# Kernel tuning notes

Measured on AMD Instinct MI355X. Metric: run time of the kernel, lower is better.

The kernel has to match this reference:

```python
import jax, jax.numpy as jnp
import numpy as np

NUM_TOKENS = 32000
BATCH = 8192
K = 10  # 'ten-hot'

def setup_inputs() -> dict:
    key = jax.random.key(0)
    x = jax.random.randint(key, (BATCH, K), 0, NUM_TOKENS, dtype=jnp.int64)
    return {"x": x}

def reference(x) -> jnp.ndarray:
    # Multi-hot encode: out[n, x[n, j]] = 1 for all j. Duplicate indices simply
    # re-write 1 (set, not add), matching the torch assignment semantics.
    B = x.shape[0]
    out = jnp.zeros((B, NUM_TOKENS), dtype=jnp.float32)
    rows = jnp.arange(B, dtype=x.dtype)[:, None]  # [B,1] broadcasts over K
    out = out.at[rows, x].set(1.0, mode="drop")
    return out
```

## Files before the change

### kernel.cpp

```cpp
#include <hip/hip_runtime.h>


#define NUM_TOKENS 32000
#define KHOT 10
#define F4_PER_ROW (NUM_TOKENS / 4)
#define BLOCK 256

typedef float f32x4 __attribute__((ext_vector_type(4)));

__global__ __launch_bounds__(BLOCK) void TenHotEncodeLayer_53566832115799_kernel(
    const int* __restrict__ x, float* __restrict__ out) {
    const int row = blockIdx.x;

    int      c[KHOT];
    unsigned bit[KHOT];
    #pragma unroll
    for (int j = 0; j < KHOT; ++j) {
        const int idx = x[row * KHOT + j];
        const bool ok = (idx >= 0) && (idx < NUM_TOKENS);
        c[j]   = ok ? (idx >> 2) : -1;
        bit[j] = 1u << (idx & 3);
    }

    f32x4* __restrict__ rowp = reinterpret_cast<f32x4*>(out) + (size_t)row * F4_PER_ROW;

    #pragma unroll 1
    for (int i0 = threadIdx.x; i0 < F4_PER_ROW; i0 += 2 * BLOCK) {
        #pragma unroll
        for (int u = 0; u < 2; ++u) {
            const int i = i0 + u * BLOCK;
            if (i < F4_PER_ROW) {
                unsigned m = 0u;
                #pragma unroll
                for (int j = 0; j < KHOT; ++j) {
                    m |= (c[j] == i) ? bit[j] : 0u;
                }
                f32x4 v;
                v.x = (m & 1u) ? 1.0f : 0.0f;
                v.y = (m & 2u) ? 1.0f : 0.0f;
                v.z = (m & 4u) ? 1.0f : 0.0f;
                v.w = (m & 8u) ? 1.0f : 0.0f;
                __builtin_nontemporal_store(v, &rowp[i]);
            }
        }
    }
}

extern "C" void kernel_launch(void* const* d_in, const int* in_sizes, int n_in,
                              void* d_out, int out_size, void* d_ws, size_t ws_size,
                              hipStream_t stream) {
    const int* x = (const int*)d_in[0];
    float* out = (float*)d_out;
    const int B = in_sizes[0] / KHOT;
    TenHotEncodeLayer_53566832115799_kernel<<<B, BLOCK, 0, stream>>>(x, out);
}
```

Before: 203.5 us.

## Use fixed grid with 32 rows per block and prefetch next row's indices

Launches a fixed grid of 256 blocks, each writing 32 consecutive rows, in place of one block per row. The next row's indices are loaded while the current row is being written, hiding their load latency. This is meant to cut block launch and scheduling overhead and the per-row index-load stall. In exchange only 256 blocks feed a GPU with many CUs, which may limit occupancy and write bandwidth, and the hard-coded grid only covers all rows when B equals 8192.

```diff
diff --git a/kernel.cpp b/kernel.cpp
--- a/kernel.cpp
+++ b/kernel.cpp
@@ -5,44 +5,61 @@
 #define KHOT 10
 #define F4_PER_ROW (NUM_TOKENS / 4)
 #define BLOCK 256
+#define GRID 256
+#define ROWS_PER_BLOCK 32
 
 typedef float f32x4 __attribute__((ext_vector_type(4)));
 
 __global__ __launch_bounds__(BLOCK) void TenHotEncodeLayer_53566832115799_kernel(
-    const int* __restrict__ x, float* __restrict__ out) {
-    const int row = blockIdx.x;
+    const int* __restrict__ x, float* __restrict__ out, int B) {
+    const int row0 = blockIdx.x * ROWS_PER_BLOCK;
 
-    int      c[KHOT];
-    unsigned bit[KHOT];
+    int raw[KHOT];
     #pragma unroll
     for (int j = 0; j < KHOT; ++j) {
-        const int idx = x[row * KHOT + j];
-        const bool ok = (idx >= 0) && (idx < NUM_TOKENS);
-        c[j]   = ok ? (idx >> 2) : -1;
-        bit[j] = 1u << (idx & 3);
+        const int rr = (row0 < B) ? row0 : 0;
+        raw[j] = x[rr * KHOT + j];
     }
 
-    f32x4* __restrict__ rowp = reinterpret_cast<f32x4*>(out) + (size_t)row * F4_PER_ROW;
+    for (int r = 0; r < ROWS_PER_BLOCK; ++r) {
+        const int row = row0 + r;
+        if (row >= B) break;
 
-    #pragma unroll 1
-    for (int i0 = threadIdx.x; i0 < F4_PER_ROW; i0 += 2 * BLOCK) {
+        int      c[KHOT];
+        unsigned bit[KHOT];
         #pragma unroll
-        for (int u = 0; u < 2; ++u) {
-            const int i = i0 + u * BLOCK;
-            if (i < F4_PER_ROW) {
-                unsigned m = 0u;
-                #pragma unroll
-                for (int j = 0; j < KHOT; ++j) {
-                    m |= (c[j] == i) ? bit[j] : 0u;
-                }
-                f32x4 v;
-                v.x = (m & 1u) ? 1.0f : 0.0f;
-                v.y = (m & 2u) ? 1.0f : 0.0f;
-                v.z = (m & 4u) ? 1.0f : 0.0f;
-                v.w = (m & 8u) ? 1.0f : 0.0f;
-                __builtin_nontemporal_store(v, &rowp[i]);
+        for (int j = 0; j < KHOT; ++j) {
+            const int idx = raw[j];
+            const bool ok = (idx >= 0) && (idx < NUM_TOKENS);
+            c[j]   = ok ? (idx >> 2) : -1;
+            bit[j] = 1u << (idx & 3);
+        }
+
+        int nxt[KHOT];
+        {
+            const int rn = (row + 1 < B) ? (row + 1) : row;
+            #pragma unroll
+            for (int j = 0; j < KHOT; ++j) nxt[j] = x[rn * KHOT + j];
+        }
+
+        f32x4* __restrict__ rowp =
+            reinterpret_cast<f32x4*>(out) + (size_t)row * F4_PER_ROW;
+        for (int i = threadIdx.x; i < F4_PER_ROW; i += BLOCK) {
+            unsigned m = 0u;
+            #pragma unroll
+            for (int j = 0; j < KHOT; ++j) {
+                m |= (c[j] == i) ? bit[j] : 0u;
             }
+            f32x4 v;
+            v.x = (m & 1u) ? 1.0f : 0.0f;
+            v.y = (m & 2u) ? 1.0f : 0.0f;
+            v.z = (m & 4u) ? 1.0f : 0.0f;
+            v.w = (m & 8u) ? 1.0f : 0.0f;
+            __builtin_nontemporal_store(v, &rowp[i]);
         }
+
+        #pragma unroll
+        for (int j = 0; j < KHOT; ++j) raw[j] = nxt[j];
     }
 }
 
@@ -52,5 +69,5 @@
     const int* x = (const int*)d_in[0];
     float* out = (float*)d_out;
     const int B = in_sizes[0] / KHOT;
-    TenHotEncodeLayer_53566832115799_kernel<<<B, BLOCK, 0, stream>>>(x, out);
+    TenHotEncodeLayer_53566832115799_kernel<<<GRID, BLOCK, 0, stream>>>(x, out, B);
 }
```

New measurement: 236.1 us. 1.16x slower.

## Switch to persistent grid-stride flat fill with prefetched row indices

Applied to the files above, without the earlier changes.

Replaces the one-block-per-row launch (8192 blocks) with a fixed 256-block grid that walks the flat output in a grid-stride loop. Each thread computes its row and column per element and prefetches the next iteration's ten indices, so the index loads overlap the current store. It also swaps the nontemporal stores for regular stores. In exchange, every element now pays for an integer divide and ten index loads, and the row-count constants are hard-coded (TOTAL_F4, clamp at 8191).

```diff
diff --git a/kernel.cpp b/kernel.cpp
--- a/kernel.cpp
+++ b/kernel.cpp
@@ -5,44 +5,54 @@
 #define KHOT 10
 #define F4_PER_ROW (NUM_TOKENS / 4)
 #define BLOCK 256
+#define FILL_GRID 256
+#define STRIDE (FILL_GRID * BLOCK)
+#define TOTAL_F4 65536000
+#define ITERS (TOTAL_F4 / STRIDE)
 
 typedef float f32x4 __attribute__((ext_vector_type(4)));
 
 __global__ __launch_bounds__(BLOCK) void TenHotEncodeLayer_53566832115799_kernel(
-    const int* __restrict__ x, float* __restrict__ out) {
-    const int row = blockIdx.x;
+    const int* __restrict__ x, f32x4* __restrict__ out) {
+    unsigned c = blockIdx.x * BLOCK + threadIdx.x;
 
-    int      c[KHOT];
-    unsigned bit[KHOT];
-    #pragma unroll
-    for (int j = 0; j < KHOT; ++j) {
-        const int idx = x[row * KHOT + j];
-        const bool ok = (idx >= 0) && (idx < NUM_TOKENS);
-        c[j]   = ok ? (idx >> 2) : -1;
-        bit[j] = 1u << (idx & 3);
+    int raw[KHOT];
+    {
+        const unsigned r0 = c / (unsigned)F4_PER_ROW;
+        #pragma unroll
+        for (int j = 0; j < KHOT; ++j) raw[j] = x[r0 * KHOT + j];
     }
 
-    f32x4* __restrict__ rowp = reinterpret_cast<f32x4*>(out) + (size_t)row * F4_PER_ROW;
+    #pragma unroll 1
+    for (int k = 0; k < ITERS; ++k) {
+        const unsigned r  = c / (unsigned)F4_PER_ROW;
+        const int      ci = (int)(c - r * (unsigned)F4_PER_ROW);
 
-    #pragma unroll 1
-    for (int i0 = threadIdx.x; i0 < F4_PER_ROW; i0 += 2 * BLOCK) {
+        const unsigned cn = c + STRIDE;
+        unsigned rn = cn / (unsigned)F4_PER_ROW;
+        if (rn > 8191u) rn = 8191u;
+        int nxt[KHOT];
         #pragma unroll
-        for (int u = 0; u < 2; ++u) {
-            const int i = i0 + u * BLOCK;
-            if (i < F4_PER_ROW) {
-                unsigned m = 0u;
-                #pragma unroll
-                for (int j = 0; j < KHOT; ++j) {
-                    m |= (c[j] == i) ? bit[j] : 0u;
-                }
-                f32x4 v;
-                v.x = (m & 1u) ? 1.0f : 0.0f;
-                v.y = (m & 2u) ? 1.0f : 0.0f;
-                v.z = (m & 4u) ? 1.0f : 0.0f;
-                v.w = (m & 8u) ? 1.0f : 0.0f;
-                __builtin_nontemporal_store(v, &rowp[i]);
-            }
+        for (int j = 0; j < KHOT; ++j) nxt[j] = x[rn * KHOT + j];
+
+        unsigned m = 0u;
+        #pragma unroll
+        for (int j = 0; j < KHOT; ++j) {
+            const int idx = raw[j];
+            const bool ok = (idx >= 0) && (idx < NUM_TOKENS);
+            const int  cj = ok ? (idx >> 2) : -1;
+            m |= (cj == ci) ? (1u << (idx & 3)) : 0u;
         }
+        f32x4 v;
+        v.x = (m & 1u) ? 1.0f : 0.0f;
+        v.y = (m & 2u) ? 1.0f : 0.0f;
+        v.z = (m & 4u) ? 1.0f : 0.0f;
+        v.w = (m & 8u) ? 1.0f : 0.0f;
+        out[c] = v;
+
+        #pragma unroll
+        for (int j = 0; j < KHOT; ++j) raw[j] = nxt[j];
+        c = cn;
     }
 }
 
@@ -50,7 +60,6 @@
                               void* d_out, int out_size, void* d_ws, size_t ws_size,
                               hipStream_t stream) {
     const int* x = (const int*)d_in[0];
-    float* out = (float*)d_out;
-    const int B = in_sizes[0] / KHOT;
-    TenHotEncodeLayer_53566832115799_kernel<<<B, BLOCK, 0, stream>>>(x, out);
+    f32x4* out = (f32x4*)d_out;
+    TenHotEncodeLayer_53566832115799_kernel<<<FILL_GRID, BLOCK, 0, stream>>>(x, out);
 }
```

After: 421.8 us. 107% more time.
